# Kernel optimization log

Hardware: AMD Instinct MI355X
Metric: run time of the kernel (lower is better)

The kernel has to match this reference:

```python
import jax, jax.numpy as jnp
import numpy as np


def _conv2d(x, w, b):
    # x: [B,C,H,W], w: [O,I,kh,kw] (SAME padding, stride 1)
    y = jax.lax.conv_general_dilated(x, w, (1, 1), 'SAME',
                                     dimension_numbers=('NCHW', 'OIHW', 'NCHW'))
    return y + b[None, :, None, None]


def _conv1x1(x, w, b):
    # w: [O,C], b: [O]
    return jnp.einsum('oc,bchw->bohw', w, x) + b[None, :, None, None]


def _attention(xq, xkv, w, b):
    # w: [3,C,C] (q,k,v), b: [3,C]. Tokens = spatial positions, features = channels.
    B, C, H, W = xq.shape
    q = _conv1x1(xq, w[0], b[0]).reshape(B, C, H * W).transpose(0, 2, 1)   # [B,HW,C]
    k = _conv1x1(xkv, w[1], b[1]).reshape(B, C, H * W).transpose(0, 2, 1)
    v = _conv1x1(xkv, w[2], b[2]).reshape(B, C, H * W).transpose(0, 2, 1)
    scale = 1.0 / jnp.sqrt(jnp.asarray(C, xq.dtype))  # d_k = channels
    a = jax.nn.softmax(jnp.einsum('bnc,bmc->bnm', q, k) * scale, axis=-1)  # [B,HW,HW]
    out = jnp.einsum('bnm,bmc->bnc', a, v).transpose(0, 2, 1).reshape(B, C, H, W)
    return out + xq


def _cell(x, h, c, w, b):
    gates = _conv2d(jnp.concatenate([x, h], axis=1), w, b)
    i, f, o, g = jnp.split(gates, 4, axis=1)
    i, f, o, g = jax.nn.sigmoid(i), jax.nn.sigmoid(f), jax.nn.sigmoid(o), jnp.tanh(g)
    c_new = f * c + i * g
    h_new = o * jnp.tanh(c_new)
    return h_new, c_new


def setup_inputs() -> dict:
    key = jax.random.key(0)
    ks = iter(jax.random.split(key, 32))
    B, T, Cin, H, W = 2, 3, 1, 32, 32
    HID, L, K, OUT = 64, 2, 3, 1
    s = 0.02
    d = {
        'x1_seq': jax.random.normal(next(ks), (B, T, Cin, H, W), jnp.float32),
        'x2_seq': jax.random.normal(next(ks), (B, T, Cin, H, W), jnp.float32),
        # ConvLSTM gate convs: layer0 in = Cin+HID, layer1 in = 2*HID, per stream
        'conv1_w0': jax.random.normal(next(ks), (4 * HID, Cin + HID, K, K)) * s,
        'conv1_b0': jnp.zeros((4 * HID,)),
        'conv1_w1': jax.random.normal(next(ks), (4 * HID, 2 * HID, K, K)) * s,
        'conv1_b1': jnp.zeros((4 * HID,)),
        'conv2_w0': jax.random.normal(next(ks), (4 * HID, Cin + HID, K, K)) * s,
        'conv2_b0': jnp.zeros((4 * HID,)),
        'conv2_w1': jax.random.normal(next(ks), (4 * HID, 2 * HID, K, K)) * s,
        'conv2_b1': jnp.zeros((4 * HID,)),
        # attention 1x1 convs, stacked [L, 3(q/k/v), HID, HID]
        'sah_w': jax.random.normal(next(ks), (L, 3, HID, HID)) * s,
        'sah_b': jnp.zeros((L, 3, HID)),
        'sac_w': jax.random.normal(next(ks), (L, 3, HID, HID)) * s,
        'sac_b': jnp.zeros((L, 3, HID)),
        'cah_w': jax.random.normal(next(ks), (L, 3, HID, HID)) * s,
        'cah_b': jnp.zeros((L, 3, HID)),
        'cac_w': jax.random.normal(next(ks), (L, 3, HID, HID)) * s,
        'cac_b': jnp.zeros((L, 3, HID)),
        # decoder
        'dec_w1': jax.random.normal(next(ks), (HID, HID, 3, 3)) * s,
        'dec_b1': jnp.zeros((HID,)),
        'dec_w2': jax.random.normal(next(ks), (OUT, HID, 3, 3)) * s,
        'dec_b2': jnp.zeros((OUT,)),
        'future_steps': 4,
    }
    return d


def reference(x1_seq, x2_seq,
              conv1_w0, conv1_b0, conv1_w1, conv1_b1,
              conv2_w0, conv2_b0, conv2_w1, conv2_b1,
              sah_w, sah_b, sac_w, sac_b, cah_w, cah_b, cac_w, cac_b,
              dec_w1, dec_b1, dec_w2, dec_b2, future_steps):
    B, T, _, H, W = x1_seq.shape
    HID = sah_w.shape[-1]
    L = sah_w.shape[0]
    cw1 = [(conv1_w0, conv1_b0), (conv1_w1, conv1_b1)]
    cw2 = [(conv2_w0, conv2_b0), (conv2_w1, conv2_b1)]

    def decoder(h):
        return _conv2d(jax.nn.relu(_conv2d(h, dec_w1, dec_b1)), dec_w2, dec_b2)

    z = jnp.zeros((B, HID, H, W), x1_seq.dtype)
    h1s, c1s = [z] * L, [z] * L
    h2s, c2s = [z] * L, [z] * L

    def step(x1_t, x2_t, h1s, c1s, h2s, c2s):
        h1s, c1s, h2s, c2s = list(h1s), list(c1s), list(h2s), list(c2s)
        for l in range(L):
            h1, c1 = _cell(x1_t, h1s[l], c1s[l], *cw1[l])
            h2, c2 = _cell(x2_t, h2s[l], c2s[l], *cw2[l])
            h1 = _attention(h1, h1, sah_w[l], sah_b[l])
            c1 = _attention(c1, c1, sac_w[l], sac_b[l])
            h2 = _attention(h2, h2, sah_w[l], sah_b[l])
            c2 = _attention(c2, c2, sac_w[l], sac_b[l])
            tag_h1, tag_c1 = h1, c1
            h1 = _attention(h1, h2, cah_w[l], cah_b[l])
            c1 = _attention(c1, c2, cac_w[l], cac_b[l])
            h2 = _attention(h2, tag_h1, cah_w[l], cah_b[l])
            c2 = _attention(c2, tag_c1, cac_w[l], cac_b[l])
            h1s[l], c1s[l], h2s[l], c2s[l] = h1, c1, h2, c2
            x1_t, x2_t = h1, h2
        return h1s, c1s, h2s, c2s

    warm1, warm2 = [], []
    for t in range(T):
        h1s, c1s, h2s, c2s = step(x1_seq[:, t], x2_seq[:, t], h1s, c1s, h2s, c2s)
        if t < T - 1:
            warm1.append(h1s[-1])
            warm2.append(h2s[-1])
    pred_warm1 = jnp.stack([decoder(h) for h in warm1], axis=1)
    pred_warm2 = jnp.stack([decoder(h) for h in warm2], axis=1)

    preds1, preds2 = [], []
    for _ in range(int(future_steps)):
        p1 = decoder(h1s[-1])
        p2 = decoder(h2s[-1])
        preds1.append(p1)
        preds2.append(p2)
        h1s, c1s, h2s, c2s = step(p1, p2, h1s, c1s, h2s, c2s)
    preds1 = jnp.stack(preds1, axis=1)
    preds2 = jnp.stack(preds2, axis=1)
    return preds1, preds2, pred_warm1, pred_warm2
```

## Files before the change

### kernel.cpp

```cpp
#include <hip/hip_runtime.h>
#include <math.h>

#define BB 2
#define HIDC 64
#define HWN 1024

typedef _Float16 half8 __attribute__((ext_vector_type(8)));
typedef float f32x4 __attribute__((ext_vector_type(4)));

static __device__ __forceinline__ unsigned short f2h_bits(float v) {
  _Float16 h = (_Float16)v;
  return __builtin_bit_cast(unsigned short, h);
}
static __device__ __forceinline__ float h_back(float v) {
  _Float16 h = (_Float16)v;
  return (float)h;
}

struct TWArgs { const float* src; float* dst; };

__global__ __launch_bounds__(256) void transpose_w(TWArgs a) {
  const int n = 576 * 64;
  for (int i = blockIdx.x * 256 + threadIdx.x; i < n; i += gridDim.x * 256) {
    int oc = i & 63, tt = i >> 6;
    a.dst[i] = a.src[(size_t)oc * 576 + tt];
  }
}

struct WSArgs { const float* src[4]; unsigned short* dh[4]; unsigned short* dl[4]; int ct[4]; };

__global__ __launch_bounds__(256) void wsplit(WSArgs a) {
  const int arr = blockIdx.y;
  const float* s = a.src[arr];
  unsigned short* dh = a.dh[arr];
  unsigned short* dl = a.dl[arr];
  const int CTc = a.ct[arr];
  const int n = 9 * 256 * 128;
  for (int i = blockIdx.x * 256 + threadIdx.x; i < n; i += gridDim.x * 256) {
    int t = i >> 15;
    int rem = i & 32767;
    int oc = rem >> 7, c = rem & 127;
    float v = (c < CTc) ? s[((size_t)oc * CTc + c) * 9 + t] : 0.f;
    dh[i] = f2h_bits(v);
    dl[i] = f2h_bits(v - h_back(v));
  }
}

struct CellArgs {
  const float* x[2]; long xbs;
  const float* h[2]; const float* c[2];
  const unsigned short* wh[2]; const unsigned short* wl[2];
  const float* bias[2];
  float* ho[2]; float* co[2];
};

template<int CX>
__global__ __launch_bounds__(256) void cell_mfma(CellArgs a) {
  constexpr int CT = CX + HIDC;
  constexpr int NCHE = (CT + 31) / 32;
  __shared__ unsigned short sBh[60 * 128];
  __shared__ unsigned short sBl[60 * 128];
  const int tile = blockIdx.x;
  const int b = blockIdx.y, st = blockIdx.z;
  const int ty0 = (tile >> 2) * 4, tx0 = (tile & 3) * 8;
  const float* xp = a.x[st] + (size_t)b * a.xbs;
  const float* hp = a.h[st] + (size_t)b * HIDC * HWN;

  for (int j = threadIdx.x; j < 6 * 128; j += 256) {
    int y = j >> 7, c = j & 127;
    int gy = ty0 - 1 + y;
    bool cok = (c < CT) && ((unsigned)gy < 32u);
    const float* srcp = (c < CX) ? (xp + (size_t)c * HWN)
                                 : (hp + (size_t)(c < CT ? (c - CX) : 0) * HWN);
#pragma unroll
    for (int x = 0; x < 10; ++x) {
      int gx = tx0 - 1 + x;
      float v = 0.f;
      if (cok && (unsigned)gx < 32u) v = srcp[gy * 32 + gx];
      int row = y * 10 + x;
      int idx = row * 128 + ((((c >> 3) ^ (row & 7)) << 3) | (c & 7));
      sBh[idx] = f2h_bits(v);
      sBl[idx] = f2h_bits(v - h_back(v));
    }
  }
  __syncthreads();

  const int w = threadIdx.x >> 6, lane = threadIdx.x & 63;
  const int g = lane >> 4, col = lane & 15;
  f32x4 acc[4][2];
#pragma unroll
  for (int gt = 0; gt < 4; ++gt) { acc[gt][0] = (f32x4)0.f; acc[gt][1] = (f32x4)0.f; }
  const unsigned short* whp = a.wh[st];
  const unsigned short* wlp = a.wl[st];

  for (int sh = 0; sh < 9; ++sh) {
    const int ky = sh / 3, kx = sh - ky * 3;
#pragma unroll
    for (int ch = 0; ch < NCHE; ++ch) {
      half8 ahf[4], alf[4];
#pragma unroll
      for (int gt = 0; gt < 4; ++gt) {
        int oc = (gt * 4 + w) * 16 + col;
        size_t off = (((size_t)sh * 256 + oc) << 7) + ch * 32 + g * 8;
        ahf[gt] = *(const half8*)&whp[off];
        alf[gt] = *(const half8*)&wlp[off];
      }
#pragma unroll
      for (int pt = 0; pt < 2; ++pt) {
        int py = pt * 2 + (col >> 3), pxx = col & 7;
        int row = (py + ky) * 10 + pxx + kx;
        int idx = row * 128 + (((ch * 4 + g) ^ (row & 7)) << 3);
        half8 bh = *(const half8*)&sBh[idx];
        half8 bl = *(const half8*)&sBl[idx];
#pragma unroll
        for (int gt = 0; gt < 4; ++gt) {
          f32x4 d = acc[gt][pt];
          d = __builtin_amdgcn_mfma_f32_16x16x32_f16(ahf[gt], bh, d, 0, 0, 0);
          d = __builtin_amdgcn_mfma_f32_16x16x32_f16(ahf[gt], bl, d, 0, 0, 0);
          d = __builtin_amdgcn_mfma_f32_16x16x32_f16(alf[gt], bh, d, 0, 0, 0);
          acc[gt][pt] = d;
        }
      }
    }
  }

  const float* cp = a.c[st] + (size_t)b * HIDC * HWN;
  float* hop = a.ho[st] + (size_t)b * HIDC * HWN;
  float* cop = a.co[st] + (size_t)b * HIDC * HWN;
  const float* bias = a.bias[st];
#pragma unroll
  for (int r = 0; r < 4; ++r) {
    const int hc = w * 16 + g * 4 + r;
    const float bi = bias[hc], bf = bias[hc + 64];
    const float bo = bias[hc + 128], bg = bias[hc + 192];
#pragma unroll
    for (int pt = 0; pt < 2; ++pt) {
      float gi = acc[0][pt][r] + bi;
      float gf = acc[1][pt][r] + bf;
      float go = acc[2][pt][r] + bo;
      float gg = acc[3][pt][r] + bg;
      gi = 1.f / (1.f + expf(-gi));
      gf = 1.f / (1.f + expf(-gf));
      go = 1.f / (1.f + expf(-go));
      gg = tanhf(gg);
      int py = pt * 2 + (col >> 3), pxx = col & 7;
      int off = hc * HWN + (ty0 + py) * 32 + tx0 + pxx;
      float cn = gf * cp[off] + gi * gg;
      cop[off] = cn;
      hop[off] = go * tanhf(cn);
    }
  }
}

struct QkvArgs {
  const float* xq[4]; const float* xkv[4];
  const float* w[4]; const float* bias[4];
  unsigned short *Qh, *Ql, *Kh, *Kl, *Vth, *Vtl;
};

__global__ __launch_bounds__(256) void qkv_kernel(QkvArgs a) {
  __shared__ float sWt[64 * 68];
  const int ptile = blockIdx.x, b = blockIdx.y;
  const int attn = blockIdx.z / 3, proj = blockIdx.z % 3;
  const float* x = (proj == 0 ? a.xq[attn] : a.xkv[attn]) + (size_t)b * HIDC * HWN;
  const float* w = a.w[attn] + proj * 64 * 64;
  const float* bias = a.bias[attn] + proj * 64;
  const size_t bb = (size_t)attn * BB + b;
  for (int i = threadIdx.x; i < 4096; i += 256) {
    int o = i >> 6, c = i & 63;
    sWt[c * 68 + o] = w[i];
  }
  __syncthreads();
  const int pq = threadIdx.x & 63, og = threadIdx.x >> 6;
  const int p0 = ptile * 64 + pq;
  float acc[16];
#pragma unroll
  for (int k = 0; k < 16; ++k) acc[k] = bias[og * 16 + k];
  for (int c = 0; c < 64; ++c) {
    float xv = x[c * HWN + p0];
#pragma unroll
    for (int k = 0; k < 16; k += 4) {
      float4 wv = *(const float4*)&sWt[c * 68 + og * 16 + k];
      acc[k+0] += xv * wv.x; acc[k+1] += xv * wv.y;
      acc[k+2] += xv * wv.z; acc[k+3] += xv * wv.w;
    }
  }
  if (proj <= 1) {
    const float sc = (proj == 0) ? 0.125f : 1.f;
    unsigned short* dh = (proj == 0 ? a.Qh : a.Kh) + (bb << 16) + p0 * 64 + og * 16;
    unsigned short* dl = (proj == 0 ? a.Ql : a.Kl) + (bb << 16) + p0 * 64 + og * 16;
#pragma unroll
    for (int k = 0; k < 16; k += 2) {
      float v0 = acc[k] * sc, v1 = acc[k+1] * sc;
      unsigned short h0 = f2h_bits(v0), h1 = f2h_bits(v1);
      *(unsigned int*)&dh[k] = (unsigned int)h0 | ((unsigned int)h1 << 16);
      unsigned short l0 = f2h_bits(v0 - h_back(v0)), l1 = f2h_bits(v1 - h_back(v1));
      *(unsigned int*)&dl[k] = (unsigned int)l0 | ((unsigned int)l1 << 16);
    }
  } else {
    unsigned short* dvh = a.Vth + (bb << 16);
    unsigned short* dvl = a.Vtl + (bb << 16);
#pragma unroll
    for (int k = 0; k < 16; ++k) {
      float v = acc[k];
      dvh[(size_t)(og * 16 + k) * HWN + p0] = f2h_bits(v);
      dvl[(size_t)(og * 16 + k) * HWN + p0] = f2h_bits(v - h_back(v));
    }
  }
}

struct AttnPArgs {
  const unsigned short *Qh, *Ql, *Kh, *Kl, *Vth, *Vtl;
  float* pbuf;
};

__global__ __launch_bounds__(256) void attn_part(AttnPArgs a) {
  __shared__ unsigned short sP[4][2][16][72];
  const int qt = blockIdx.x >> 2, ks = blockIdx.x & 3;
  const int b = blockIdx.y, at = blockIdx.z;
  const size_t bb = (size_t)at * BB + b;
  const int tid = threadIdx.x;
  const int w = tid >> 6, lane = tid & 63;
  const int g = lane >> 4, qc = lane & 15;
  const int swz = (qc & 7) << 3;
  const unsigned short* Qhp = a.Qh + (bb << 16);
  const unsigned short* Qlp = a.Ql + (bb << 16);
  const unsigned short* Khp = a.Kh + (bb << 16);
  const unsigned short* Klp = a.Kl + (bb << 16);
  const unsigned short* Vhp = a.Vth + (bb << 16);
  const unsigned short* Vlp = a.Vtl + (bb << 16);

  const int qrow = qt * 64 + w * 16 + qc;
  const half8 bqh0 = *(const half8*)&Qhp[qrow * 64 + 0  + g * 8];
  const half8 bqh1 = *(const half8*)&Qhp[qrow * 64 + 32 + g * 8];
  const half8 bql0 = *(const half8*)&Qlp[qrow * 64 + 0  + g * 8];
  const half8 bql1 = *(const half8*)&Qlp[qrow * 64 + 32 + g * 8];

  float mrun = -1e30f, lrun = 0.f;
  f32x4 sO[4];
#pragma unroll
  for (int i = 0; i < 4; ++i) sO[i] = (f32x4)0.f;

  for (int kk = 0; kk < 4; ++kk) {
    const int jt = (ks * 4 + kk) * 64;
    f32x4 sS[4];
#pragma unroll
    for (int i = 0; i < 4; ++i) sS[i] = (f32x4)0.f;
#pragma unroll
    for (int sb = 0; sb < 4; ++sb) {
      const int j = jt + sb * 16 + qc;
      const half8 ah0 = *(const half8*)&Khp[j * 64 + 0  + g * 8];
      const half8 ah1 = *(const half8*)&Khp[j * 64 + 32 + g * 8];
      const half8 al0 = *(const half8*)&Klp[j * 64 + 0  + g * 8];
      const half8 al1 = *(const half8*)&Klp[j * 64 + 32 + g * 8];
      f32x4 d = sS[sb];
      d = __builtin_amdgcn_mfma_f32_16x16x32_f16(ah0, bqh0, d, 0, 0, 0);
      d = __builtin_amdgcn_mfma_f32_16x16x32_f16(ah1, bqh1, d, 0, 0, 0);
      d = __builtin_amdgcn_mfma_f32_16x16x32_f16(ah0, bql0, d, 0, 0, 0);
      d = __builtin_amdgcn_mfma_f32_16x16x32_f16(ah1, bql1, d, 0, 0, 0);
      d = __builtin_amdgcn_mfma_f32_16x16x32_f16(al0, bqh0, d, 0, 0, 0);
      d = __builtin_amdgcn_mfma_f32_16x16x32_f16(al1, bqh1, d, 0, 0, 0);
      sS[sb] = d;
    }
    float mt = -1e30f;
#pragma unroll
    for (int sb = 0; sb < 4; ++sb)
#pragma unroll
      for (int r = 0; r < 4; ++r) mt = fmaxf(mt, sS[sb][r]);
    mt = fmaxf(mt, __shfl_xor(mt, 16));
    mt = fmaxf(mt, __shfl_xor(mt, 32));
    const float mn = fmaxf(mrun, mt);
    const float al = __expf(mrun - mn);
    float p[16];
    float ps = 0.f;
#pragma unroll
    for (int sb = 0; sb < 4; ++sb)
#pragma unroll
      for (int r = 0; r < 4; ++r) {
        float e = __expf(sS[sb][r] - mn);
        p[sb * 4 + r] = e; ps += e;
      }
    ps += __shfl_xor(ps, 16);
    ps += __shfl_xor(ps, 32);
    lrun = lrun * al + ps;
    mrun = mn;
#pragma unroll
    for (int i = 0; i < 4; ++i) {
      sO[i][0] *= al; sO[i][1] *= al; sO[i][2] *= al; sO[i][3] *= al;
    }
#pragma unroll
    for (int sb = 0; sb < 4; ++sb)
#pragma unroll
      for (int rp = 0; rp < 4; rp += 2) {
        int j = sb * 16 + g * 4 + rp;
        int js = j ^ swz;
        float v0 = p[sb * 4 + rp], v1 = p[sb * 4 + rp + 1];
        unsigned short h0 = f2h_bits(v0), h1 = f2h_bits(v1);
        *(unsigned int*)&sP[w][0][qc][js] = (unsigned int)h0 | ((unsigned int)h1 << 16);
        unsigned short l0 = f2h_bits(v0 - h_back(v0)), l1 = f2h_bits(v1 - h_back(v1));
        *(unsigned int*)&sP[w][1][qc][js] = (unsigned int)l0 | ((unsigned int)l1 << 16);
      }
    const half8 ph0 = *(const half8*)&sP[w][0][qc][((0 + g) ^ (qc & 7)) * 8];
    const half8 ph1 = *(const half8*)&sP[w][0][qc][((4 + g) ^ (qc & 7)) * 8];
    const half8 pl0 = *(const half8*)&sP[w][1][qc][((0 + g) ^ (qc & 7)) * 8];
    const half8 pl1 = *(const half8*)&sP[w][1][qc][((4 + g) ^ (qc & 7)) * 8];
#pragma unroll
    for (int vs = 0; vs < 4; ++vs) {
      const int vc = vs * 16 + qc;
      const half8 vh0 = *(const half8*)&Vhp[(size_t)vc * HWN + jt + 0  + g * 8];
      const half8 vh1 = *(const half8*)&Vhp[(size_t)vc * HWN + jt + 32 + g * 8];
      const half8 vl0 = *(const half8*)&Vlp[(size_t)vc * HWN + jt + 0  + g * 8];
      const half8 vl1 = *(const half8*)&Vlp[(size_t)vc * HWN + jt + 32 + g * 8];
      f32x4 d = sO[vs];
      d = __builtin_amdgcn_mfma_f32_16x16x32_f16(vh0, ph0, d, 0, 0, 0);
      d = __builtin_amdgcn_mfma_f32_16x16x32_f16(vh1, ph1, d, 0, 0, 0);
      d = __builtin_amdgcn_mfma_f32_16x16x32_f16(vh0, pl0, d, 0, 0, 0);
      d = __builtin_amdgcn_mfma_f32_16x16x32_f16(vh1, pl1, d, 0, 0, 0);
      d = __builtin_amdgcn_mfma_f32_16x16x32_f16(vl0, ph0, d, 0, 0, 0);
      d = __builtin_amdgcn_mfma_f32_16x16x32_f16(vl1, ph1, d, 0, 0, 0);
      sO[vs] = d;
    }
  }
  float* pb = a.pbuf + ((bb * 16 + qt) * 4 + ks) * 4224;
  const int qloc = w * 16 + qc;
#pragma unroll
  for (int vs = 0; vs < 4; ++vs)
#pragma unroll
    for (int r = 0; r < 4; ++r)
      pb[qloc * 64 + vs * 16 + g * 4 + r] = sO[vs][r];
  if (g == 0) {
    pb[4096 + qloc] = mrun;
    pb[4160 + qloc] = lrun;
  }
}

struct AttnMArgs { const float* pbuf; const float* xq[4]; float* out[4]; };

__global__ __launch_bounds__(256) void attn_merge(AttnMArgs a) {
  __shared__ float sW[4][64];
  __shared__ float sL[64];
  const int qt = blockIdx.x, b = blockIdx.y, at = blockIdx.z;
  const float* pb = a.pbuf + (((size_t)at * BB + b) * 16 + qt) * 4 * 4224;
  if (threadIdx.x < 64) {
    int r = threadIdx.x;
    float mm[4];
#pragma unroll
    for (int i = 0; i < 4; ++i) mm[i] = pb[i * 4224 + 4096 + r];
    float M = fmaxf(fmaxf(mm[0], mm[1]), fmaxf(mm[2], mm[3]));
    float L = 0.f;
#pragma unroll
    for (int i = 0; i < 4; ++i) {
      float wv = __expf(mm[i] - M);
      sW[i][r] = wv;
      L += pb[i * 4224 + 4160 + r] * wv;
    }
    sL[r] = L;
  }
  __syncthreads();
  const int c = threadIdx.x >> 2, rg = (threadIdx.x & 3) * 16;
  const float* xq = a.xq[at] + (size_t)b * HIDC * HWN;
  float* op = a.out[at] + (size_t)b * HIDC * HWN;
  const int p0 = qt * 64 + rg;
#pragma unroll
  for (int rr4 = 0; rr4 < 16; rr4 += 4) {
    float rv[4];
#pragma unroll
    for (int k = 0; k < 4; ++k) {
      int r = rg + rr4 + k;
      float acc = 0.f;
#pragma unroll
      for (int i = 0; i < 4; ++i) acc += pb[i * 4224 + r * 64 + c] * sW[i][r];
      rv[k] = acc / sL[r];
    }
    float4 x4 = *(const float4*)&xq[(size_t)c * HWN + p0 + rr4];
    float4 res; res.x = rv[0] + x4.x; res.y = rv[1] + x4.y;
    res.z = rv[2] + x4.z; res.w = rv[3] + x4.w;
    *(float4*)&op[(size_t)c * HWN + p0 + rr4] = res;
  }
}

struct Dec1Args { const float* in[2]; const float* w; const float* b; float* tmp; };

__global__ __launch_bounds__(512) void dec1_kernel(Dec1Args a) {
  __shared__ float sIn[64 * 48];
  __shared__ float sHa[64 * 17];
  __shared__ float sHb[64 * 17];
  const int tile = blockIdx.x, b = blockIdx.y, st = blockIdx.z;
  const int ty0 = (tile >> 3) << 2, tx0 = (tile & 7) << 2;
  const float* ip = a.in[st] + (size_t)b * HIDC * HWN;
  for (int idx = threadIdx.x; idx < 64 * 36; idx += 512) {
    int ic = idx / 36, pos = idx - ic * 36;
    int iy = pos / 6, ix = pos - iy * 6;
    int gy = ty0 - 1 + iy, gx = tx0 - 1 + ix;
    float v = 0.f;
    if ((unsigned)gy < 32u && (unsigned)gx < 32u) v = ip[ic * HWN + gy * 32 + gx];
    sIn[ic * 48 + iy * 8 + ix] = v;
  }
  __syncthreads();
  const int oc = threadIdx.x & 63, ps = (threadIdx.x >> 6) & 3;
  const int hh = threadIdx.x >> 8;
  const int icb = hh * 32, ice = icb + 32;
  float acc0 = 0.f, acc1 = 0.f, acc2 = 0.f, acc3 = 0.f;
  const float* wp = a.w;
  for (int ic = icb; ic < ice; ++ic) {
    float w9[9];
#pragma unroll
    for (int t = 0; t < 9; ++t) w9[t] = wp[(ic * 9 + t) * 64 + oc];
    float in[18];
#pragma unroll
    for (int ry = 0; ry < 3; ++ry) {
      float4 v4 = *(const float4*)&sIn[ic * 48 + (ps + ry) * 8];
      float2 v2 = *(const float2*)&sIn[ic * 48 + (ps + ry) * 8 + 4];
      in[ry*6+0]=v4.x; in[ry*6+1]=v4.y; in[ry*6+2]=v4.z; in[ry*6+3]=v4.w;
      in[ry*6+4]=v2.x; in[ry*6+5]=v2.y;
    }
#pragma unroll
    for (int ky = 0; ky < 3; ++ky)
#pragma unroll
      for (int kx = 0; kx < 3; ++kx) {
        float wv = w9[ky * 3 + kx];
        acc0 += wv * in[ky * 6 + kx + 0];
        acc1 += wv * in[ky * 6 + kx + 1];
        acc2 += wv * in[ky * 6 + kx + 2];
        acc3 += wv * in[ky * 6 + kx + 3];
      }
  }
  float* sH = hh ? sHb : sHa;
  sH[oc * 17 + ps * 4 + 0] = acc0;
  sH[oc * 17 + ps * 4 + 1] = acc1;
  sH[oc * 17 + ps * 4 + 2] = acc2;
  sH[oc * 17 + ps * 4 + 3] = acc3;
  __syncthreads();
  float* dst = a.tmp + ((size_t)st * BB + b) * HIDC * HWN;
  for (int idx = threadIdx.x; idx < 1024; idx += 512) {
    int oc2 = idx >> 4, p = idx & 15;
    float v = sHa[oc2 * 17 + p] + sHb[oc2 * 17 + p] + a.b[oc2];
    v = fmaxf(v, 0.f);
    dst[(size_t)oc2 * HWN + (ty0 + (p >> 2)) * 32 + tx0 + (p & 3)] = v;
  }
}

struct Dec2Args { const float* tmp; const float* w; const float* b;
                  float* dst0; float* dst1; long bstr; };

__global__ __launch_bounds__(256) void dec2_kernel(Dec2Args a) {
  __shared__ float sIn[64 * 48];
  __shared__ float sW[64 * 9];
  const int tile = blockIdx.x, b = blockIdx.y, st = blockIdx.z;
  const int ty0 = (tile >> 3) << 2, tx0 = (tile & 7) << 2;
  const float* ip = a.tmp + ((size_t)st * BB + b) * HIDC * HWN;
  for (int idx = threadIdx.x; idx < 64 * 36; idx += 256) {
    int ic = idx / 36, pos = idx - ic * 36;
    int iy = pos / 6, ix = pos - iy * 6;
    int gy = ty0 - 1 + iy, gx = tx0 - 1 + ix;
    float v = 0.f;
    if ((unsigned)gy < 32u && (unsigned)gx < 32u) v = ip[ic * HWN + gy * 32 + gx];
    sIn[ic * 48 + iy * 8 + ix] = v;
  }
  for (int idx = threadIdx.x; idx < 576; idx += 256) sW[idx] = a.w[idx];
  __syncthreads();
  const int px = threadIdx.x >> 4, icg = threadIdx.x & 15;
  const int py = px >> 2, pxx = px & 3;
  float acc = 0.f;
#pragma unroll
  for (int i = 0; i < 4; ++i) {
    int ic = icg * 4 + i;
    const float* row = &sIn[ic * 48];
    const float* wv = &sW[ic * 9];
#pragma unroll
    for (int ky = 0; ky < 3; ++ky)
#pragma unroll
      for (int kx = 0; kx < 3; ++kx)
        acc += wv[ky * 3 + kx] * row[(py + ky) * 8 + pxx + kx];
  }
#pragma unroll
  for (int d = 1; d < 16; d <<= 1) acc += __shfl_xor(acc, d);
  if (icg == 0) {
    float* d = (st == 0 ? a.dst0 : a.dst1);
    d[(size_t)b * a.bstr + (ty0 + py) * 32 + tx0 + pxx] = acc + a.b[0];
  }
}

extern "C" void kernel_launch(void* const* d_in, const int* in_sizes, int n_in,
                              void* d_out, int out_size, void* d_ws, size_t ws_size,
                              hipStream_t stream) {
  (void)in_sizes; (void)n_in; (void)out_size; (void)ws_size;
  const float* x1_seq = (const float*)d_in[0];
  const float* x2_seq = (const float*)d_in[1];
  const float* c1w[2] = {(const float*)d_in[2], (const float*)d_in[4]};
  const float* c1b[2] = {(const float*)d_in[3], (const float*)d_in[5]};
  const float* c2w[2] = {(const float*)d_in[6], (const float*)d_in[8]};
  const float* c2b[2] = {(const float*)d_in[7], (const float*)d_in[9]};
  const float* sah_w = (const float*)d_in[10]; const float* sah_b = (const float*)d_in[11];
  const float* sac_w = (const float*)d_in[12]; const float* sac_b = (const float*)d_in[13];
  const float* cah_w = (const float*)d_in[14]; const float* cah_b = (const float*)d_in[15];
  const float* cac_w = (const float*)d_in[16]; const float* cac_b = (const float*)d_in[17];
  const float* dw1 = (const float*)d_in[18]; const float* db1 = (const float*)d_in[19];
  const float* dw2 = (const float*)d_in[20]; const float* db2 = (const float*)d_in[21];
  float* out = (float*)d_out;
  float* ws = (float*)d_ws;

  const size_t SPL = (size_t)BB * HIDC * HWN;
  float* h1s = ws;
  float* c1s = h1s + 2 * SPL;
  float* h2s = c1s + 2 * SPL;
  float* c2s = h2s + 2 * SPL;
  float* hc1 = c2s + 2 * SPL;
  float* cc1 = hc1 + SPL;
  float* hc2 = cc1 + SPL;
  float* cc2 = hc2 + SPL;
  float* hs1 = cc2 + SPL;
  float* cs1 = hs1 + SPL;
  float* hs2 = cs1 + SPL;
  float* cs2 = hs2 + SPL;
  float* Qf  = cs2 + SPL;
  float* Kf  = Qf + 4 * SPL;
  float* Vf  = Kf + 4 * SPL;
  unsigned short* Qh = (unsigned short*)Qf;  unsigned short* Ql = Qh + (size_t)8 * 65536;
  unsigned short* Kh = (unsigned short*)Kf;  unsigned short* Kl = Kh + (size_t)8 * 65536;
  unsigned short* Vth = (unsigned short*)Vf; unsigned short* Vtl = Vth + (size_t)8 * 65536;
  float* dtmp = Vf + 4 * SPL;
  float* pbuf = dtmp + 2 * SPL;
  float* wsb  = pbuf + (size_t)4 * BB * 16 * 4 * 4224;
  unsigned short* wsp = (unsigned short*)wsb;
  const size_t WN = (size_t)9 * 256 * 128;
  float* wtd = wsb + (8 * WN) / 2;

  hipMemsetAsync(ws, 0, 8 * SPL * sizeof(float), stream);

  const dim3 blk(256);
  const dim3 blk2(512);

  {
    TWArgs tw; tw.src = dw1; tw.dst = wtd;
    transpose_w<<<dim3(32), blk, 0, stream>>>(tw);
    WSArgs wsa;
    wsa.src[0] = c1w[0]; wsa.ct[0] = 65;
    wsa.src[1] = c1w[1]; wsa.ct[1] = 128;
    wsa.src[2] = c2w[0]; wsa.ct[2] = 65;
    wsa.src[3] = c2w[1]; wsa.ct[3] = 128;
    for (int i = 0; i < 4; ++i) {
      wsa.dh[i] = wsp + i * WN;
      wsa.dl[i] = wsp + (4 + i) * WN;
    }
    wsplit<<<dim3(64, 4), blk, 0, stream>>>(wsa);
  }

  auto attn_stage = [&](const float* q0, const float* q1, const float* q2, const float* q3,
                        const float* k0, const float* k1, const float* k2, const float* k3,
                        const float* wh, const float* bh, const float* wc, const float* bc,
                        float* o0, float* o1, float* o2, float* o3) {
    QkvArgs qa;
    qa.xq[0]=q0; qa.xq[1]=q1; qa.xq[2]=q2; qa.xq[3]=q3;
    qa.xkv[0]=k0; qa.xkv[1]=k1; qa.xkv[2]=k2; qa.xkv[3]=k3;
    qa.w[0]=wh; qa.w[1]=wc; qa.w[2]=wh; qa.w[3]=wc;
    qa.bias[0]=bh; qa.bias[1]=bc; qa.bias[2]=bh; qa.bias[3]=bc;
    qa.Qh=Qh; qa.Ql=Ql; qa.Kh=Kh; qa.Kl=Kl; qa.Vth=Vth; qa.Vtl=Vtl;
    qkv_kernel<<<dim3(16, BB, 12), blk, 0, stream>>>(qa);
    AttnPArgs ap; ap.Qh=Qh; ap.Ql=Ql; ap.Kh=Kh; ap.Kl=Kl; ap.Vth=Vth; ap.Vtl=Vtl;
    ap.pbuf=pbuf;
    attn_part<<<dim3(64, BB, 4), blk, 0, stream>>>(ap);
    AttnMArgs am; am.pbuf=pbuf;
    am.xq[0]=q0; am.xq[1]=q1; am.xq[2]=q2; am.xq[3]=q3;
    am.out[0]=o0; am.out[1]=o1; am.out[2]=o2; am.out[3]=o3;
    attn_merge<<<dim3(16, BB, 4), blk, 0, stream>>>(am);
  };

  auto decode = [&](long off1, long off2, long bstr) {
    Dec1Args d1; d1.in[0] = h1s + SPL; d1.in[1] = h2s + SPL;
    d1.w = wtd; d1.b = db1; d1.tmp = dtmp;
    dec1_kernel<<<dim3(64, BB, 2), blk2, 0, stream>>>(d1);
    Dec2Args d2; d2.tmp = dtmp; d2.w = dw2; d2.b = db2;
    d2.dst0 = out + off1; d2.dst1 = out + off2; d2.bstr = bstr;
    dec2_kernel<<<dim3(64, BB, 2), blk, 0, stream>>>(d2);
  };

  for (int s = 0; s < 6; ++s) {
    const float *x1, *x2; long xbs;
    if (s < 3) { x1 = x1_seq + s * HWN; x2 = x2_seq + s * HWN; xbs = 3 * HWN; }
    else       { x1 = out + (s - 3) * HWN; x2 = out + 8192 + (s - 3) * HWN; xbs = 4 * HWN; }

    for (int l = 0; l < 2; ++l) {
      if (l == 1) { x1 = h1s; x2 = h2s; xbs = (long)HIDC * HWN; }
      CellArgs ca;
      ca.x[0] = x1; ca.x[1] = x2; ca.xbs = xbs;
      ca.h[0] = h1s + l * SPL; ca.h[1] = h2s + l * SPL;
      ca.c[0] = c1s + l * SPL; ca.c[1] = c2s + l * SPL;
      ca.wh[0] = wsp + (l == 0 ? 0 : 1) * WN;
      ca.wh[1] = wsp + (l == 0 ? 2 : 3) * WN;
      ca.wl[0] = wsp + (4 + (l == 0 ? 0 : 1)) * WN;
      ca.wl[1] = wsp + (4 + (l == 0 ? 2 : 3)) * WN;
      ca.bias[0] = c1b[l]; ca.bias[1] = c2b[l];
      ca.ho[0] = hc1; ca.ho[1] = hc2; ca.co[0] = cc1; ca.co[1] = cc2;
      if (l == 0) cell_mfma<1><<<dim3(32, BB, 2), blk, 0, stream>>>(ca);
      else        cell_mfma<64><<<dim3(32, BB, 2), blk, 0, stream>>>(ca);

      attn_stage(hc1, cc1, hc2, cc2,
                 hc1, cc1, hc2, cc2,
                 sah_w + l * 12288, sah_b + l * 192,
                 sac_w + l * 12288, sac_b + l * 192,
                 hs1, cs1, hs2, cs2);
      attn_stage(hs1, cs1, hs2, cs2,
                 hs2, cs2, hs1, cs1,
                 cah_w + l * 12288, cah_b + l * 192,
                 cac_w + l * 12288, cac_b + l * 192,
                 h1s + l * SPL, c1s + l * SPL, h2s + l * SPL, c2s + l * SPL);
    }

    if (s == 0)      decode(16384,        20480,        2048);
    else if (s == 1) decode(16384 + 1024, 20480 + 1024, 2048);
    else             decode((s - 2) * HWN, 8192 + (s - 2) * HWN, 4096);
  }
}
```

Before: 2.107 ms.

## Halve ConvLSTM cell tile size to double block count and reorder weight layout

Measured after the change: 2.158 ms. +2.4%, slower.

```diff
diff --git a/kernel.cpp b/kernel.cpp
--- a/kernel.cpp
+++ b/kernel.cpp
@@ -35,12 +35,14 @@
   unsigned short* dh = a.dh[arr];
   unsigned short* dl = a.dl[arr];
   const int CTc = a.ct[arr];
-  const int n = 9 * 256 * 128;
+  const int n = 9 * 4 * 256 * 32;
   for (int i = blockIdx.x * 256 + threadIdx.x; i < n; i += gridDim.x * 256) {
-    int t = i >> 15;
-    int rem = i & 32767;
-    int oc = rem >> 7, c = rem & 127;
-    float v = (c < CTc) ? s[((size_t)oc * CTc + c) * 9 + t] : 0.f;
+    int cl = i & 31;
+    int oc = (i >> 5) & 255;
+    int chunk = (i >> 13) & 3;
+    int sh = i >> 15;
+    int c = chunk * 32 + cl;
+    float v = (c < CTc) ? s[((size_t)oc * CTc + c) * 9 + sh] : 0.f;
     dh[i] = f2h_bits(v);
     dl[i] = f2h_bits(v - h_back(v));
   }
@@ -58,69 +60,61 @@
 __global__ __launch_bounds__(256) void cell_mfma(CellArgs a) {
   constexpr int CT = CX + HIDC;
   constexpr int NCHE = (CT + 31) / 32;
-  __shared__ unsigned short sBh[60 * 128];
-  __shared__ unsigned short sBl[60 * 128];
+  constexpr int NIT = 9 * NCHE;
+  __shared__ unsigned short sBh[36 * 128];
+  __shared__ unsigned short sBl[36 * 128];
   const int tile = blockIdx.x;
   const int b = blockIdx.y, st = blockIdx.z;
-  const int ty0 = (tile >> 2) * 4, tx0 = (tile & 3) * 8;
+  const int ty0 = (tile >> 3) << 2, tx0 = (tile & 7) << 2;
   const float* xp = a.x[st] + (size_t)b * a.xbs;
   const float* hp = a.h[st] + (size_t)b * HIDC * HWN;
 
-  for (int j = threadIdx.x; j < 6 * 128; j += 256) {
-    int y = j >> 7, c = j & 127;
-    int gy = ty0 - 1 + y;
-    bool cok = (c < CT) && ((unsigned)gy < 32u);
-    const float* srcp = (c < CX) ? (xp + (size_t)c * HWN)
-                                 : (hp + (size_t)(c < CT ? (c - CX) : 0) * HWN);
-#pragma unroll
-    for (int x = 0; x < 10; ++x) {
-      int gx = tx0 - 1 + x;
-      float v = 0.f;
-      if (cok && (unsigned)gx < 32u) v = srcp[gy * 32 + gx];
-      int row = y * 10 + x;
-      int idx = row * 128 + ((((c >> 3) ^ (row & 7)) << 3) | (c & 7));
-      sBh[idx] = f2h_bits(v);
-      sBl[idx] = f2h_bits(v - h_back(v));
-    }
+  for (int idx = threadIdx.x; idx < 36 * 128; idx += 256) {
+    int row = idx >> 7, c = idx & 127;
+    int y = row / 6, x = row - y * 6;
+    int gy = ty0 - 1 + y, gx = tx0 - 1 + x;
+    float v = 0.f;
+    if (c < CT && (unsigned)gy < 32u && (unsigned)gx < 32u)
+      v = (c < CX) ? xp[(size_t)c * HWN + gy * 32 + gx]
+                   : hp[(size_t)(c - CX) * HWN + gy * 32 + gx];
+    int di = row * 128 + ((((c >> 3) ^ (row & 7)) << 3) | (c & 7));
+    sBh[di] = f2h_bits(v);
+    sBl[di] = f2h_bits(v - h_back(v));
   }
   __syncthreads();
 
   const int w = threadIdx.x >> 6, lane = threadIdx.x & 63;
   const int g = lane >> 4, col = lane & 15;
-  f32x4 acc[4][2];
-#pragma unroll
-  for (int gt = 0; gt < 4; ++gt) { acc[gt][0] = (f32x4)0.f; acc[gt][1] = (f32x4)0.f; }
+  const int py = col >> 2, pxx = col & 3;
+  f32x4 acc[4];
+#pragma unroll
+  for (int gt = 0; gt < 4; ++gt) acc[gt] = (f32x4)0.f;
   const unsigned short* whp = a.wh[st];
   const unsigned short* wlp = a.wl[st];
 
-  for (int sh = 0; sh < 9; ++sh) {
+#pragma unroll
+  for (int it = 0; it < NIT; ++it) {
+    const int sh = it / NCHE, ch = it - sh * NCHE;
     const int ky = sh / 3, kx = sh - ky * 3;
-#pragma unroll
-    for (int ch = 0; ch < NCHE; ++ch) {
-      half8 ahf[4], alf[4];
-#pragma unroll
-      for (int gt = 0; gt < 4; ++gt) {
-        int oc = (gt * 4 + w) * 16 + col;
-        size_t off = (((size_t)sh * 256 + oc) << 7) + ch * 32 + g * 8;
-        ahf[gt] = *(const half8*)&whp[off];
-        alf[gt] = *(const half8*)&wlp[off];
-      }
-#pragma unroll
-      for (int pt = 0; pt < 2; ++pt) {
-        int py = pt * 2 + (col >> 3), pxx = col & 7;
-        int row = (py + ky) * 10 + pxx + kx;
-        int idx = row * 128 + (((ch * 4 + g) ^ (row & 7)) << 3);
-        half8 bh = *(const half8*)&sBh[idx];
-        half8 bl = *(const half8*)&sBl[idx];
-#pragma unroll
-        for (int gt = 0; gt < 4; ++gt) {
-          f32x4 d = acc[gt][pt];
-          d = __builtin_amdgcn_mfma_f32_16x16x32_f16(ahf[gt], bh, d, 0, 0, 0);
-          d = __builtin_amdgcn_mfma_f32_16x16x32_f16(ahf[gt], bl, d, 0, 0, 0);
-          d = __builtin_amdgcn_mfma_f32_16x16x32_f16(alf[gt], bh, d, 0, 0, 0);
-          acc[gt][pt] = d;
-        }
-      }
+    half8 ah[4], al[4];
+#pragma unroll
+    for (int gt = 0; gt < 4; ++gt) {
+      const int oc = (gt * 4 + w) * 16 + col;
+      const size_t off = ((size_t)(sh * 4 + ch) * 256 + oc) * 32 + g * 8;
+      ah[gt] = *(const half8*)&whp[off];
+      al[gt] = *(const half8*)&wlp[off];
+    }
+    const int row = (py + ky) * 6 + (pxx + kx);
+    const int bi = row * 128 + (((ch * 4 + g) ^ (row & 7)) << 3);
+    const half8 bh = *(const half8*)&sBh[bi];
+    const half8 bl = *(const half8*)&sBl[bi];
+#pragma unroll
+    for (int gt = 0; gt < 4; ++gt) {
+      f32x4 d = acc[gt];
+      d = __builtin_amdgcn_mfma_f32_16x16x32_f16(ah[gt], bh, d, 0, 0, 0);
+      d = __builtin_amdgcn_mfma_f32_16x16x32_f16(ah[gt], bl, d, 0, 0, 0);
+      d = __builtin_amdgcn_mfma_f32_16x16x32_f16(al[gt], bh, d, 0, 0, 0);
+      acc[gt] = d;
     }
   }
 
@@ -131,24 +125,18 @@
 #pragma unroll
   for (int r = 0; r < 4; ++r) {
     const int hc = w * 16 + g * 4 + r;
-    const float bi = bias[hc], bf = bias[hc + 64];
-    const float bo = bias[hc + 128], bg = bias[hc + 192];
-#pragma unroll
-    for (int pt = 0; pt < 2; ++pt) {
-      float gi = acc[0][pt][r] + bi;
-      float gf = acc[1][pt][r] + bf;
-      float go = acc[2][pt][r] + bo;
-      float gg = acc[3][pt][r] + bg;
-      gi = 1.f / (1.f + expf(-gi));
-      gf = 1.f / (1.f + expf(-gf));
-      go = 1.f / (1.f + expf(-go));
-      gg = tanhf(gg);
-      int py = pt * 2 + (col >> 3), pxx = col & 7;
-      int off = hc * HWN + (ty0 + py) * 32 + tx0 + pxx;
-      float cn = gf * cp[off] + gi * gg;
-      cop[off] = cn;
-      hop[off] = go * tanhf(cn);
-    }
+    float gi = acc[0][r] + bias[hc];
+    float gf = acc[1][r] + bias[hc + 64];
+    float go = acc[2][r] + bias[hc + 128];
+    float gg = acc[3][r] + bias[hc + 192];
+    gi = 1.f / (1.f + expf(-gi));
+    gf = 1.f / (1.f + expf(-gf));
+    go = 1.f / (1.f + expf(-go));
+    gg = tanhf(gg);
+    int off = hc * HWN + (ty0 + py) * 32 + tx0 + pxx;
+    float cn = gf * cp[off] + gi * gg;
+    cop[off] = cn;
+    hop[off] = go * tanhf(cn);
   }
 }
 
@@ -523,7 +511,7 @@
   float* pbuf = dtmp + 2 * SPL;
   float* wsb  = pbuf + (size_t)4 * BB * 16 * 4 * 4224;
   unsigned short* wsp = (unsigned short*)wsb;
-  const size_t WN = (size_t)9 * 256 * 128;
+  const size_t WN = (size_t)9 * 4 * 256 * 32;
   float* wtd = wsb + (8 * WN) / 2;
 
   hipMemsetAsync(ws, 0, 8 * SPL * sizeof(float), stream);
@@ -592,8 +580,8 @@
       ca.wl[1] = wsp + (4 + (l == 0 ? 2 : 3)) * WN;
       ca.bias[0] = c1b[l]; ca.bias[1] = c2b[l];
       ca.ho[0] = hc1; ca.ho[1] = hc2; ca.co[0] = cc1; ca.co[1] = cc2;
-      if (l == 0) cell_mfma<1><<<dim3(32, BB, 2), blk, 0, stream>>>(ca);
-      else        cell_mfma<64><<<dim3(32, BB, 2), blk, 0, stream>>>(ca);
+      if (l == 0) cell_mfma<1><<<dim3(64, BB, 2), blk, 0, stream>>>(ca);
+      else        cell_mfma<64><<<dim3(64, BB, 2), blk, 0, stream>>>(ca);
 
       attn_stage(hc1, cc1, hc2, cc2,
                  hc1, cc1, hc2, cc2,
```
